# Performance work log

Hardware: AMD Instinct MI355X
Metric: run time of the kernel (lower is better)

Reference implementation:

```python
import jax, jax.numpy as jnp
import numpy as np

B, F, CTX, HID, L, NB = 16384, 64, 128, 512, 8, 2


def setup_inputs() -> dict:
    key = jax.random.key(0)
    ks = jax.random.split(key, 8)
    inputs = jax.random.normal(ks[0], (B, F), jnp.float32)
    context = jax.random.normal(ks[1], (B, CTX), jnp.float32)
    n_id = F // 2                      # identity features per coupling layer
    in_dim = n_id + CTX                # coupling net input = identity half + context
    out_dim = F                        # 2 * num_transform_features (shift | scale)
    s_in = 1.0 / np.sqrt(in_dim)
    s_h = 1.0 / np.sqrt(HID)
    W_in = jax.random.uniform(ks[2], (L, in_dim, HID), jnp.float32, -s_in, s_in)
    b_in = jax.random.uniform(ks[3], (L, HID), jnp.float32, -s_in, s_in)
    W_h = jax.random.uniform(ks[4], (L, NB, HID, HID), jnp.float32, -s_h, s_h)
    b_h = jax.random.uniform(ks[5], (L, NB, HID), jnp.float32, -s_h, s_h)
    # output layer init: normal(0, 0.01) weight, zero bias (as in torch source)
    W_out = 0.01 * jax.random.normal(ks[6], (L, HID, out_dim), jnp.float32)
    b_out = jnp.zeros((L, out_dim), jnp.float32)
    # fixed random permutations between coupling layers (nflows RandomPermutation buffers)
    rng = np.random.RandomState(42)
    perms = jnp.asarray(np.stack([rng.permutation(F) for _ in range(L - 1)]), jnp.int32)
    return dict(inputs=inputs, context=context, W_in=W_in, b_in=b_in,
                W_h=W_h, b_h=b_h, W_out=W_out, b_out=b_out, perms=perms)


def reference(inputs, context, W_in, b_in, W_h, b_h, W_out, b_out, perms):
    F_ = inputs.shape[-1]
    n_layers = W_in.shape[0]
    n_blocks = W_h.shape[1]
    nt = F_ // 2  # num transform features
    even_idx = jnp.arange(0, F_, 2)
    odd_idx = jnp.arange(1, F_, 2)
    x = jnp.clip(inputs, -1.0, 1.0)
    logdet = jnp.zeros(x.shape[0], x.dtype)
    for i in range(n_layers):
        # mask[::2]=1 for even layers -> mask>0 (even indices) are TRANSFORM features
        if i % 2 == 0:
            t_idx, id_idx = even_idx, odd_idx
        else:
            t_idx, id_idx = odd_idx, even_idx
        id_split = x[:, id_idx]   # [B, nt]
        tr_split = x[:, t_idx]    # [B, nt]
        h = jax.nn.relu(jnp.concatenate([id_split, context], -1) @ W_in[i] + b_in[i])
        for j in range(n_blocks):
            h = jax.nn.relu(h @ W_h[i, j] + b_h[i, j])
        p = h @ W_out[i] + b_out[i]            # [B, 2*nt]
        shift = p[:, :nt]
        scale = jax.nn.sigmoid(p[:, nt:] + 2.0) + 1e-3
        logdet = logdet + jnp.sum(jnp.log(scale), axis=-1)
        x = x.at[:, t_idx].set(tr_split * scale + shift).at[:, id_idx].set(id_split)
        if i < n_layers - 1:
            x = x[:, perms[i]]
    return jnp.clip(x, -1.0, 1.0), logdet
```

## Files before the change

### kernel.cpp

```cpp
#include <hip/hip_runtime.h>


typedef float v4f  __attribute__((ext_vector_type(4)));
typedef float v16f __attribute__((ext_vector_type(16)));
typedef int   v4i  __attribute__((ext_vector_type(4)));
typedef int   v8i  __attribute__((ext_vector_type(8)));
typedef unsigned char uchar;
typedef unsigned long long ull;

#define BATCH 16384
#define NF    64
#define NCTX  128
#define NL    8

#define RS     528
#define HHALF  256
#define AST    208
#define AHALF  96
#define PST    68

#define WSCALE     16.0f
#define WSCALE_INV 0.0625f

#define WIN_EPL   (192 * 512)
#define WH_EPB    (512 * 512)
#define WOUT_EPL  (512 * 64)
#define OFF_WIN   ((size_t)0)
#define OFF_WH    ((size_t)(8 * WIN_EPL))
#define OFF_WOUT  (OFF_WH + (size_t)(16 * WH_EPB))
#define TOT_PACK_ELEMS (OFF_WOUT + (size_t)(8 * WOUT_EPL))
#define NEED_WS   (TOT_PACK_ELEMS)

template<bool HI>
__device__ __forceinline__ unsigned int pk2(float a, float b, unsigned int old) {
    return __builtin_amdgcn_cvt_pk_fp8_f32(a, b, old, HI);
}
__device__ __forceinline__ uchar q8(float v) {
    return (uchar)(__builtin_amdgcn_cvt_pk_fp8_f32(v, v, 0u, false) & 0xffu);
}

__global__ void pack_weights_kernel(const float* __restrict__ W_in,
                                    const float* __restrict__ W_h,
                                    const float* __restrict__ W_out,
                                    unsigned char* __restrict__ ws) {
    const int TIN  = 8 * (WIN_EPL / 8);
    const int TH   = 16 * (WH_EPB / 8);
    const int TOUT = 8 * (WOUT_EPL / 8);
    int t = blockIdx.x * blockDim.x + threadIdx.x;
    if (t >= TIN + TH + TOUT) return;
    float v[8];
    if (t < TIN + TH) {
        const float* src; int r, rawK;
        if (t < TIN) {
            int i = t / (WIN_EPL / 8); r = t - i * (WIN_EPL / 8);
            src = W_in + (size_t)i * (160 * 512); rawK = 160;
        } else {
            int u = t - TIN; int ij = u >> 15; r = u & 32767;
            src = W_h + (size_t)ij * WH_EPB; rawK = 512;
        }
        int kb  = r >> 12, rem = r & 4095;
        int ls  = rem >> 2, g = rem & 3;
        int lane = ls & 63;
        int n = (ls >> 6) * 32 + (lane & 31);
        int pig = (g == 1) ? 2 : (g == 2) ? 1 : g;
        int k0 = kb * 64 + (lane >> 5) * 32 + pig * 8;
#pragma unroll
        for (int j = 0; j < 8; ++j) {
            int k = k0 + j;
            v[j] = (k < rawK) ? src[(size_t)k * 512 + n] * WSCALE : 0.f;
        }
    } else {
        int u = t - TIN - TH;
        int i = u >> 12, r = u & 4095;
        const float* src = W_out + (size_t)i * WOUT_EPL;
        int frag = r >> 6, lane = r & 63;
        int k0 = (frag >> 2) * 32 + (lane >> 4) * 8;
        int n  = (frag & 3) * 16 + (lane & 15);
#pragma unroll
        for (int j = 0; j < 8; ++j)
            v[j] = src[(size_t)(k0 + j) * 64 + n] * WSCALE;
    }
    uint2 o;
    o.x = pk2<false>(v[0], v[1], 0u);
    o.x = pk2<true >(v[2], v[3], o.x);
    o.y = pk2<false>(v[4], v[5], 0u);
    o.y = pk2<true >(v[6], v[7], o.y);
    *(uint2*)(ws + (size_t)t * 8) = o;
}

__device__ __forceinline__ v16f mfma32(ull a, ull b, v16f c) {
    return __builtin_amdgcn_mfma_f32_32x32x16_fp8_fp8((long)a, (long)b, c, 0, 0, 0);
}
__device__ __forceinline__ v4f mfma16(ull a, ull b, v4f c) {
    return __builtin_amdgcn_mfma_f32_16x16x32_fp8_fp8((long)a, (long)b, c, 0, 0, 0);
}
__device__ __forceinline__ v16f mfma64(v8i a, v8i b, v16f c) {
    return __builtin_amdgcn_mfma_scale_f32_32x32x64_f8f6f4(
        a, b, c, 0, 0, 0, 0x7f7f7f7f, 0, 0x7f7f7f7f);
}

template<int NKB>
__device__ __forceinline__ void gemm32mx(
    const uchar* __restrict__ wpk,
    const float* __restrict__ bias,
    const uchar* __restrict__ Abuf, int ast, int halfoff,
    uchar* __restrict__ Obuf,
    int pair, int lane)
{
    const int l31 = lane & 31, hl = lane >> 5;
    v16f a00, a01, a10, a11;
#pragma unroll
    for (int r = 0; r < 16; ++r) { a00[r] = 0.f; a01[r] = 0.f;
                                   a10[r] = 0.f; a11[r] = 0.f; }
    const uchar* aLo0 = Abuf + l31 * ast + hl * 16;
    const uchar* aHi0 = aLo0 + halfoff;
    const uchar* aLo1 = aLo0 + 32 * ast;
    const uchar* aHi1 = aHi0 + 32 * ast;
    const uchar* bp = wpk + (size_t)(pair * 128 + lane) * 32;

    auto loadB = [&](int s, int kb) -> v8i {
        if (kb >= NKB) kb = NKB - 1;
        const uchar* p = bp + s * 2048 + (size_t)kb * 32768;
        v4i lo = *(const v4i*)p;
        v4i hi = *(const v4i*)(p + 16);
        return __builtin_shufflevector(lo, hi, 0, 1, 2, 3, 4, 5, 6, 7);
    };
    auto loadA = [&](const uchar* lo_, const uchar* hi_, int kb) -> v8i {
        v4i lo = *(const v4i*)(lo_ + kb * 32);
        v4i hi = *(const v4i*)(hi_ + kb * 32);
        return __builtin_shufflevector(lo, hi, 0, 1, 2, 3, 4, 5, 6, 7);
    };

    v8i b00 = loadB(0, 0), b10 = loadB(1, 0);
    v8i b01 = loadB(0, 1), b11 = loadB(1, 1);
    int kb = 0;
#pragma unroll 1
    for (; kb + 1 < NKB; kb += 2) {
        v8i x0 = loadA(aLo0, aHi0, kb);
        v8i x1 = loadA(aLo1, aHi1, kb);
        a00 = mfma64(b00, x0, a00);
        a01 = mfma64(b00, x1, a01);
        a10 = mfma64(b10, x0, a10);
        a11 = mfma64(b10, x1, a11);
        b00 = loadB(0, kb + 2); b10 = loadB(1, kb + 2);
        x0 = loadA(aLo0, aHi0, kb + 1);
        x1 = loadA(aLo1, aHi1, kb + 1);
        a00 = mfma64(b01, x0, a00);
        a01 = mfma64(b01, x1, a01);
        a10 = mfma64(b11, x0, a10);
        a11 = mfma64(b11, x1, a11);
        b01 = loadB(0, kb + 3); b11 = loadB(1, kb + 3);
    }
    if constexpr (NKB & 1) {
        v8i x0 = loadA(aLo0, aHi0, NKB - 1);
        v8i x1 = loadA(aLo1, aHi1, NKB - 1);
        a00 = mfma64(b00, x0, a00);
        a01 = mfma64(b00, x1, a01);
        a10 = mfma64(b10, x0, a10);
        a11 = mfma64(b10, x1, a11);
    }

    const uchar* ob0 = Obuf + l31 * RS + 4 * hl;
    const uchar* ob1 = ob0 + 32 * RS;
    auto emit = [&](const v16f& am0, const v16f& am1, int strip) {
#pragma unroll
        for (int q = 0; q < 4; ++q) {
            const int n0 = strip * 32 + q * 8 + 4 * hl;
            float4 bv = *(const float4*)(bias + n0);
            unsigned int u0, u1;
            u0 = pk2<false>(fmaxf(fmaf(am0[4 * q + 0], WSCALE_INV, bv.x), 0.f),
                            fmaxf(fmaf(am0[4 * q + 1], WSCALE_INV, bv.y), 0.f), 0u);
            u0 = pk2<true >(fmaxf(fmaf(am0[4 * q + 2], WSCALE_INV, bv.z), 0.f),
                            fmaxf(fmaf(am0[4 * q + 3], WSCALE_INV, bv.w), 0.f), u0);
            u1 = pk2<false>(fmaxf(fmaf(am1[4 * q + 0], WSCALE_INV, bv.x), 0.f),
                            fmaxf(fmaf(am1[4 * q + 1], WSCALE_INV, bv.y), 0.f), 0u);
            u1 = pk2<true >(fmaxf(fmaf(am1[4 * q + 2], WSCALE_INV, bv.z), 0.f),
                            fmaxf(fmaf(am1[4 * q + 3], WSCALE_INV, bv.w), 0.f), u1);
            const int g = strip * 4 + q;
            const int off = (g & 1) * HHALF + ((g >> 1) << 3);
            *(unsigned int*)(ob0 + off) = u0;
            *(unsigned int*)(ob1 + off) = u1;
        }
    };
    emit(a00, a01, pair * 2 + 0);
    emit(a10, a11, pair * 2 + 1);
}

template<int KC>
__device__ __forceinline__ void gemm32_raw(
    const float* __restrict__ wraw,
    const float* __restrict__ bias,
    const uchar* __restrict__ Abuf, int ast, int ahalf,
    uchar* __restrict__ Obuf,
    int strip, int lane)
{
    constexpr int P = KC / 2;
    const int l31 = lane & 31, hl = lane >> 5;
    v16f acc0, acc1;
#pragma unroll
    for (int r = 0; r < 16; ++r) { acc0[r] = 0.f; acc1[r] = 0.f; }
    const uchar* a0p = Abuf + l31 * ast + hl * ahalf;
    const uchar* a1p = a0p + 32 * ast;

    auto loadB = [&](int kc) -> ull {
        if (kc >= KC) kc = KC - 1;
        int n  = strip * 32 + l31;
        int k0 = kc * 16 + hl * 8;
        unsigned int lo, hi;
        lo = pk2<false>(wraw[(size_t)(k0 + 0) * 512 + n] * WSCALE,
                        wraw[(size_t)(k0 + 1) * 512 + n] * WSCALE, 0u);
        lo = pk2<true >(wraw[(size_t)(k0 + 2) * 512 + n] * WSCALE,
                        wraw[(size_t)(k0 + 3) * 512 + n] * WSCALE, lo);
        hi = pk2<false>(wraw[(size_t)(k0 + 4) * 512 + n] * WSCALE,
                        wraw[(size_t)(k0 + 5) * 512 + n] * WSCALE, 0u);
        hi = pk2<true >(wraw[(size_t)(k0 + 6) * 512 + n] * WSCALE,
                        wraw[(size_t)(k0 + 7) * 512 + n] * WSCALE, hi);
        return ((ull)hi << 32) | (ull)lo;
    };

    ull b0 = loadB(0), b1 = loadB(1), b2 = loadB(2), b3 = loadB(3);
    int p2 = 0;
#pragma unroll 1
    for (; p2 + 1 < P; p2 += 2) {
        ulonglong2 Aa0 = *(const ulonglong2*)(a0p + p2 * 16);
        ulonglong2 Aa1 = *(const ulonglong2*)(a1p + p2 * 16);
        acc0 = mfma32(Aa0.x, b0, acc0);
        acc1 = mfma32(Aa1.x, b0, acc1);
        b0 = loadB(2 * p2 + 4);
        acc0 = mfma32(Aa0.y, b1, acc0);
        acc1 = mfma32(Aa1.y, b1, acc1);
        b1 = loadB(2 * p2 + 5);
        ulonglong2 Ab0 = *(const ulonglong2*)(a0p + p2 * 16 + 16);
        ulonglong2 Ab1 = *(const ulonglong2*)(a1p + p2 * 16 + 16);
        acc0 = mfma32(Ab0.x, b2, acc0);
        acc1 = mfma32(Ab1.x, b2, acc1);
        b2 = loadB(2 * p2 + 6);
        acc0 = mfma32(Ab0.y, b3, acc0);
        acc1 = mfma32(Ab1.y, b3, acc1);
        b3 = loadB(2 * p2 + 7);
    }
    if constexpr (P & 1) {
        ulonglong2 Aa0 = *(const ulonglong2*)(a0p + (P - 1) * 16);
        ulonglong2 Aa1 = *(const ulonglong2*)(a1p + (P - 1) * 16);
        acc0 = mfma32(Aa0.x, b0, acc0);
        acc1 = mfma32(Aa1.x, b0, acc1);
        acc0 = mfma32(Aa0.y, b1, acc0);
        acc1 = mfma32(Aa1.y, b1, acc1);
    }

    const int n = strip * 32 + l31;
    const int nb = ((n >> 3) & 1) * HHALF + ((n >> 4) << 3) + (n & 7);
    const float bv = bias[n];
#pragma unroll
    for (int reg = 0; reg < 16; ++reg) {
        int row = (reg & 3) + 8 * (reg >> 2) + 4 * hl;
        float v0 = fmaxf(fmaf(acc0[reg], WSCALE_INV, bv), 0.f);
        Obuf[row * RS + nb] = q8(v0);
        float v1 = fmaxf(fmaf(acc1[reg], WSCALE_INV, bv), 0.f);
        Obuf[(row + 32) * RS + nb] = q8(v1);
    }
}

template<bool PACKED>
__device__ __forceinline__ void gemm16_out(
    const uchar* __restrict__ wpk,
    const float* __restrict__ wraw,
    const float* __restrict__ bias,
    const uchar* __restrict__ Abuf,
    float* __restrict__ Pbuf,
    int w, int lane)
{
    const int quad = lane >> 4, l15 = lane & 15;
    const int ntb  = w & 3;
    const int mtb0 = w >> 2;
    const int row0 = mtb0 * 16 + l15;
    const int row1 = row0 + 32;
    v4f acc0, acc1;
    acc0[0] = acc0[1] = acc0[2] = acc0[3] = 0.f;
    acc1[0] = acc1[1] = acc1[2] = acc1[3] = 0.f;
    const uchar* ap0 = Abuf + row0 * RS + (quad & 1) * HHALF + ((quad >> 1) << 3);
    const uchar* ap1 = Abuf + row1 * RS + (quad & 1) * HHALF + ((quad >> 1) << 3);
    const uchar* bptr =
        PACKED ? wpk + (size_t)(ntb * 64 + lane) * 8 : (const uchar*)0;
    constexpr int KC = 16;

    auto loadB = [&](int kc) -> ull {
        if (kc >= KC) kc = KC - 1;
        if constexpr (PACKED) {
            return *(const ull*)(bptr + (size_t)kc * 2048);
        } else {
            int n  = ntb * 16 + l15;
            int k0 = kc * 32 + quad * 8;
            unsigned int lo, hi;
            lo = pk2<false>(wraw[(size_t)(k0 + 0) * 64 + n] * WSCALE,
                            wraw[(size_t)(k0 + 1) * 64 + n] * WSCALE, 0u);
            lo = pk2<true >(wraw[(size_t)(k0 + 2) * 64 + n] * WSCALE,
                            wraw[(size_t)(k0 + 3) * 64 + n] * WSCALE, lo);
            hi = pk2<false>(wraw[(size_t)(k0 + 4) * 64 + n] * WSCALE,
                            wraw[(size_t)(k0 + 5) * 64 + n] * WSCALE, 0u);
            hi = pk2<true >(wraw[(size_t)(k0 + 6) * 64 + n] * WSCALE,
                            wraw[(size_t)(k0 + 7) * 64 + n] * WSCALE, hi);
            return ((ull)hi << 32) | (ull)lo;
        }
    };
    auto step = [&](int kc, ull bb) {
        ull a0 = *(const ull*)(ap0 + kc * 16);
        acc0 = mfma16(bb, a0, acc0);
        ull a1 = *(const ull*)(ap1 + kc * 16);
        acc1 = mfma16(bb, a1, acc1);
    };

    ull b0 = loadB(0), b1 = loadB(1), b2 = loadB(2), b3 = loadB(3);
    int kc = 0;
#pragma unroll 1
    for (; kc + 3 < KC; kc += 4) {
        step(kc + 0, b0); b0 = loadB(kc + 4);
        step(kc + 1, b1); b1 = loadB(kc + 5);
        step(kc + 2, b2); b2 = loadB(kc + 6);
        step(kc + 3, b3); b3 = loadB(kc + 7);
    }

    float4 bv = *(const float4*)(bias + ntb * 16 + quad * 4);
    float4 o0, o1;
    o0.x = fmaf(acc0[0], WSCALE_INV, bv.x);
    o0.y = fmaf(acc0[1], WSCALE_INV, bv.y);
    o0.z = fmaf(acc0[2], WSCALE_INV, bv.z);
    o0.w = fmaf(acc0[3], WSCALE_INV, bv.w);
    *(float4*)(Pbuf + row0 * PST + ntb * 16 + quad * 4) = o0;
    o1.x = fmaf(acc1[0], WSCALE_INV, bv.x);
    o1.y = fmaf(acc1[1], WSCALE_INV, bv.y);
    o1.z = fmaf(acc1[2], WSCALE_INV, bv.z);
    o1.w = fmaf(acc1[3], WSCALE_INV, bv.w);
    *(float4*)(Pbuf + row1 * PST + ntb * 16 + quad * 4) = o1;
}

template<bool PACKED>
__global__ __launch_bounds__(512, 2) void flow_kernel(
    const float* __restrict__ inputs,
    const float* __restrict__ ctx,
    const float* __restrict__ W_in,  const float* __restrict__ b_in,
    const float* __restrict__ W_h,   const float* __restrict__ b_h,
    const float* __restrict__ W_out, const float* __restrict__ b_out,
    const int*   __restrict__ perms,
    const uchar* __restrict__ wpk,
    float* __restrict__ out)
{
    __shared__ __align__(16) uchar hbuf0[64 * RS];
    __shared__ __align__(16) uchar hbuf1[64 * RS];
    __shared__ __align__(16) uchar abuf[64 * AST];
    __shared__ __align__(16) float xbuf[64 * NF];
    __shared__ int permsh[NF];

    float* pbuf    = (float*)hbuf1;
    float* scratch = (float*)hbuf0;

    const int tid  = threadIdx.x;
    const int wave = tid >> 6;
    const int lane = tid & 63;
    const int trow = tid >> 3;
    const int t8   = tid & 7;
    const int row0 = blockIdx.x * 64;

    {
#pragma unroll
        for (int j = 0; j < 2; ++j) {
            float4 v = ((const float4*)(inputs + (size_t)row0 * NF))[tid + j * 512];
            v.x = fminf(fmaxf(v.x, -1.f), 1.f);
            v.y = fminf(fmaxf(v.y, -1.f), 1.f);
            v.z = fminf(fmaxf(v.z, -1.f), 1.f);
            v.w = fminf(fmaxf(v.w, -1.f), 1.f);
            ((float4*)xbuf)[tid + j * 512] = v;
        }
    }
    {
        const float* crow = ctx + (size_t)(row0 + trow) * NCTX + t8 * 16;
        float4 f0 = ((const float4*)crow)[0];
        float4 f1 = ((const float4*)crow)[1];
        float4 f2 = ((const float4*)crow)[2];
        float4 f3 = ((const float4*)crow)[3];
        uint2 ck0, ck1;
        ck0.x = pk2<false>(f0.x, f0.y, 0u);
        ck0.x = pk2<true >(f0.z, f0.w, ck0.x);
        ck0.y = pk2<false>(f1.x, f1.y, 0u);
        ck0.y = pk2<true >(f1.z, f1.w, ck0.y);
        ck1.x = pk2<false>(f2.x, f2.y, 0u);
        ck1.x = pk2<true >(f2.z, f2.w, ck1.x);
        ck1.y = pk2<false>(f3.x, f3.y, 0u);
        ck1.y = pk2<true >(f3.z, f3.w, ck1.y);
        *(uint2*)(abuf + trow * AST + (2 + t8) * 8) = ck0;
        *(uint2*)(abuf + trow * AST + AHALF + (2 + t8) * 8) = ck1;
    }
    if (tid < 256) {
        int r = tid >> 2, q = tid & 3;
        *(ull*)(abuf + r * AST + (q & 1) * AHALF + 80 + ((q >> 1) << 3)) = 0ULL;
    }
    float ld_acc = 0.f;
    __syncthreads();

#pragma unroll 1
    for (int i = 0; i < NL; ++i) {
        const int par = i & 1;
        const int idp = par ^ 1;

        if (t8 < 4) {
            const float* xr = xbuf + trow * NF + idp;
            uint2 idv;
            idv.x = pk2<false>(xr[2 * (t8 * 8 + 0)], xr[2 * (t8 * 8 + 1)], 0u);
            idv.x = pk2<true >(xr[2 * (t8 * 8 + 2)], xr[2 * (t8 * 8 + 3)], idv.x);
            idv.y = pk2<false>(xr[2 * (t8 * 8 + 4)], xr[2 * (t8 * 8 + 5)], 0u);
            idv.y = pk2<true >(xr[2 * (t8 * 8 + 6)], xr[2 * (t8 * 8 + 7)], idv.y);
            *(uint2*)(abuf + trow * AST + (t8 & 1) * AHALF + ((t8 >> 1) << 3)) = idv;
        }
        __syncthreads();

        if constexpr (PACKED) {
            gemm32mx<3>(wpk + OFF_WIN + (size_t)i * WIN_EPL, b_in + i * 512,
                        abuf, AST, AHALF, hbuf0, wave, lane);
            __syncthreads();
            gemm32mx<8>(wpk + OFF_WH + (size_t)(i * 2 + 0) * WH_EPB,
                        b_h + (i * 2 + 0) * 512,
                        hbuf0, RS, HHALF, hbuf1, wave, lane);
            __syncthreads();
            gemm32mx<8>(wpk + OFF_WH + (size_t)(i * 2 + 1) * WH_EPB,
                        b_h + (i * 2 + 1) * 512,
                        hbuf1, RS, HHALF, hbuf0, wave, lane);
            __syncthreads();
        } else {
            gemm32_raw<10>(W_in + (size_t)i * (160 * 512), b_in + i * 512,
                           abuf, AST, AHALF, hbuf0, wave * 2 + 0, lane);
            gemm32_raw<10>(W_in + (size_t)i * (160 * 512), b_in + i * 512,
                           abuf, AST, AHALF, hbuf0, wave * 2 + 1, lane);
            __syncthreads();
            gemm32_raw<32>(W_h + (size_t)(i * 2 + 0) * WH_EPB,
                           b_h + (i * 2 + 0) * 512,
                           hbuf0, RS, HHALF, hbuf1, wave * 2 + 0, lane);
            gemm32_raw<32>(W_h + (size_t)(i * 2 + 0) * WH_EPB,
                           b_h + (i * 2 + 0) * 512,
                           hbuf0, RS, HHALF, hbuf1, wave * 2 + 1, lane);
            __syncthreads();
            gemm32_raw<32>(W_h + (size_t)(i * 2 + 1) * WH_EPB,
                           b_h + (i * 2 + 1) * 512,
                           hbuf1, RS, HHALF, hbuf0, wave * 2 + 0, lane);
            gemm32_raw<32>(W_h + (size_t)(i * 2 + 1) * WH_EPB,
                           b_h + (i * 2 + 1) * 512,
                           hbuf1, RS, HHALF, hbuf0, wave * 2 + 1, lane);
            __syncthreads();
        }
        gemm16_out<PACKED>(
            PACKED ? wpk + OFF_WOUT + (size_t)i * WOUT_EPL : (const uchar*)0,
            W_out + (size_t)i * WOUT_EPL, b_out + i * 64,
            hbuf0, pbuf, wave, lane);
        __syncthreads();

        {
#pragma unroll
            for (int j = 0; j < 4; ++j) {
                int sc = t8 * 4 + j;
                float shiftv = pbuf[trow * PST + sc];
                float z = pbuf[trow * PST + 32 + sc] + 2.0f;
                float s = 1.0f / (1.0f + __expf(-z)) + 0.001f;
                int tc = 2 * sc + par;
                xbuf[trow * NF + tc] = xbuf[trow * NF + tc] * s + shiftv;
                ld_acc += __logf(s);
            }
        }
        __syncthreads();

        if (i < NL - 1) {
            ((float4*)scratch)[tid]       = ((float4*)xbuf)[tid];
            ((float4*)scratch)[tid + 512] = ((float4*)xbuf)[tid + 512];
            if (tid < NF) permsh[tid] = perms[i * NF + tid];
            __syncthreads();
#pragma unroll
            for (int j = 0; j < 8; ++j) {
                int c = t8 * 8 + j;
                xbuf[trow * NF + c] = scratch[trow * NF + permsh[c]];
            }
            __syncthreads();
        }
    }

    {
#pragma unroll
        for (int j = 0; j < 2; ++j) {
            float4 v = ((float4*)xbuf)[tid + j * 512];
            v.x = fminf(fmaxf(v.x, -1.f), 1.f);
            v.y = fminf(fmaxf(v.y, -1.f), 1.f);
            v.z = fminf(fmaxf(v.z, -1.f), 1.f);
            v.w = fminf(fmaxf(v.w, -1.f), 1.f);
            ((float4*)(out + (size_t)row0 * NF))[tid + j * 512] = v;
        }
    }
    ld_acc += __shfl_down(ld_acc, 1);
    ld_acc += __shfl_down(ld_acc, 2);
    ld_acc += __shfl_down(ld_acc, 4);
    if (t8 == 0) out[(size_t)BATCH * NF + row0 + trow] = ld_acc;
}

extern "C" void kernel_launch(void* const* d_in, const int* in_sizes, int n_in,
                              void* d_out, int out_size, void* d_ws, size_t ws_size,
                              hipStream_t stream) {
    const float* inputs  = (const float*)d_in[0];
    const float* context = (const float*)d_in[1];
    const float* W_in    = (const float*)d_in[2];
    const float* b_in    = (const float*)d_in[3];
    const float* W_h     = (const float*)d_in[4];
    const float* b_h     = (const float*)d_in[5];
    const float* W_out   = (const float*)d_in[6];
    const float* b_out   = (const float*)d_in[7];
    const int*   perms   = (const int*)d_in[8];
    float* out = (float*)d_out;

    if (ws_size >= (size_t)NEED_WS) {
        uchar* ws = (uchar*)d_ws;
        const int total_threads = (int)(TOT_PACK_ELEMS / 8);
        pack_weights_kernel<<<(total_threads + 255) / 256, 256, 0, stream>>>(
            W_in, W_h, W_out, ws);
        flow_kernel<true><<<256, 512, 0, stream>>>(
            inputs, context, W_in, b_in, W_h, b_h, W_out, b_out, perms, ws, out);
    } else {
        flow_kernel<false><<<256, 512, 0, stream>>>(
            inputs, context, W_in, b_in, W_h, b_h, W_out, b_out, perms,
            (const uchar*)0, out);
    }
}
```

Measured before the change: 200.3 us.

## Fuse affine coupling epilogue into output GEMM and replace permutations with composed index table

The output GEMM is restructured so each wave computes both the shift and scale tiles for the same rows, which lets it apply the sigmoid, the affine update and the log-determinant directly in registers instead of staging them through a shared buffer. The per-layer physical permutation of xbuf (copy to scratch, gather back, two barriers) is removed. In its place a table of composed permutation indices, built once per block, is used for indirect reads and writes into xbuf. This removes several barriers and shared-memory passes per layer, at the cost of irregular gathers into xbuf and a table-building loop of up to seven chained global reads at startup.

```diff
diff --git a/kernel.cpp b/kernel.cpp
--- a/kernel.cpp
+++ b/kernel.cpp
@@ -17,7 +17,6 @@
 #define HHALF  256
 #define AST    208
 #define AHALF  96
-#define PST    68
 
 #define WSCALE     16.0f
 #define WSCALE_INV 0.0625f
@@ -262,32 +261,34 @@
 }
 
 template<bool PACKED>
-__device__ __forceinline__ void gemm16_out(
+__device__ __forceinline__ float gemm16_fused(
     const uchar* __restrict__ wpk,
     const float* __restrict__ wraw,
     const float* __restrict__ bias,
     const uchar* __restrict__ Abuf,
-    float* __restrict__ Pbuf,
-    int w, int lane)
+    float* __restrict__ xbuf,
+    const int* __restrict__ ct,
+    int par, int w, int lane)
 {
     const int quad = lane >> 4, l15 = lane & 15;
-    const int ntb  = w & 3;
-    const int mtb0 = w >> 2;
-    const int row0 = mtb0 * 16 + l15;
-    const int row1 = row0 + 32;
+    const int mtb  = w >> 1;
+    const int npair = w & 1;
+    const int ntb0 = npair, ntb1 = npair + 2;
+    const int row  = mtb * 16 + l15;
     v4f acc0, acc1;
     acc0[0] = acc0[1] = acc0[2] = acc0[3] = 0.f;
     acc1[0] = acc1[1] = acc1[2] = acc1[3] = 0.f;
-    const uchar* ap0 = Abuf + row0 * RS + (quad & 1) * HHALF + ((quad >> 1) << 3);
-    const uchar* ap1 = Abuf + row1 * RS + (quad & 1) * HHALF + ((quad >> 1) << 3);
-    const uchar* bptr =
-        PACKED ? wpk + (size_t)(ntb * 64 + lane) * 8 : (const uchar*)0;
+    const uchar* ap = Abuf + row * RS + (quad & 1) * HHALF + ((quad >> 1) << 3);
+    const uchar* bp0 =
+        PACKED ? wpk + (size_t)(ntb0 * 64 + lane) * 8 : (const uchar*)0;
+    const uchar* bp1 =
+        PACKED ? wpk + (size_t)(ntb1 * 64 + lane) * 8 : (const uchar*)0;
     constexpr int KC = 16;
 
-    auto loadB = [&](int kc) -> ull {
+    auto loadB = [&](const uchar* bp, int ntb, int kc) -> ull {
         if (kc >= KC) kc = KC - 1;
         if constexpr (PACKED) {
-            return *(const ull*)(bptr + (size_t)kc * 2048);
+            return *(const ull*)(bp + (size_t)kc * 2048);
         } else {
             int n  = ntb * 16 + l15;
             int k0 = kc * 32 + quad * 8;
@@ -303,35 +304,43 @@
             return ((ull)hi << 32) | (ull)lo;
         }
     };
-    auto step = [&](int kc, ull bb) {
-        ull a0 = *(const ull*)(ap0 + kc * 16);
-        acc0 = mfma16(bb, a0, acc0);
-        ull a1 = *(const ull*)(ap1 + kc * 16);
-        acc1 = mfma16(bb, a1, acc1);
+    auto step = [&](int kc, ull bu, ull bv_) {
+        ull a = *(const ull*)(ap + kc * 16);
+        acc0 = mfma16(bu, a, acc0);
+        acc1 = mfma16(bv_, a, acc1);
     };
 
-    ull b0 = loadB(0), b1 = loadB(1), b2 = loadB(2), b3 = loadB(3);
+    ull u0 = loadB(bp0, ntb0, 0), u1 = loadB(bp0, ntb0, 1);
+    ull u2 = loadB(bp0, ntb0, 2), u3 = loadB(bp0, ntb0, 3);
+    ull v0 = loadB(bp1, ntb1, 0), v1 = loadB(bp1, ntb1, 1);
+    ull v2 = loadB(bp1, ntb1, 2), v3 = loadB(bp1, ntb1, 3);
     int kc = 0;
 #pragma unroll 1
     for (; kc + 3 < KC; kc += 4) {
-        step(kc + 0, b0); b0 = loadB(kc + 4);
-        step(kc + 1, b1); b1 = loadB(kc + 5);
-        step(kc + 2, b2); b2 = loadB(kc + 6);
-        step(kc + 3, b3); b3 = loadB(kc + 7);
-    }
-
-    float4 bv = *(const float4*)(bias + ntb * 16 + quad * 4);
-    float4 o0, o1;
-    o0.x = fmaf(acc0[0], WSCALE_INV, bv.x);
-    o0.y = fmaf(acc0[1], WSCALE_INV, bv.y);
-    o0.z = fmaf(acc0[2], WSCALE_INV, bv.z);
-    o0.w = fmaf(acc0[3], WSCALE_INV, bv.w);
-    *(float4*)(Pbuf + row0 * PST + ntb * 16 + quad * 4) = o0;
-    o1.x = fmaf(acc1[0], WSCALE_INV, bv.x);
-    o1.y = fmaf(acc1[1], WSCALE_INV, bv.y);
-    o1.z = fmaf(acc1[2], WSCALE_INV, bv.z);
-    o1.w = fmaf(acc1[3], WSCALE_INV, bv.w);
-    *(float4*)(Pbuf + row1 * PST + ntb * 16 + quad * 4) = o1;
+        step(kc + 0, u0, v0);
+        u0 = loadB(bp0, ntb0, kc + 4); v0 = loadB(bp1, ntb1, kc + 4);
+        step(kc + 1, u1, v1);
+        u1 = loadB(bp0, ntb0, kc + 5); v1 = loadB(bp1, ntb1, kc + 5);
+        step(kc + 2, u2, v2);
+        u2 = loadB(bp0, ntb0, kc + 6); v2 = loadB(bp1, ntb1, kc + 6);
+        step(kc + 3, u3, v3);
+        u3 = loadB(bp0, ntb0, kc + 7); v3 = loadB(bp1, ntb1, kc + 7);
+    }
+
+    const int n0 = ntb0 * 16 + quad * 4;
+    float ld = 0.f;
+#pragma unroll
+    for (int r = 0; r < 4; ++r) {
+        float shiftv = fmaf(acc0[r], WSCALE_INV, bias[n0 + r]);
+        float z      = fmaf(acc1[r], WSCALE_INV, bias[32 + n0 + r]) + 2.0f;
+        float s      = 1.0f / (1.0f + __expf(-z)) + 0.001f;
+        int sc = n0 + r;
+        int tc = ct[2 * sc + par];
+        float xo = xbuf[row * NF + tc];
+        xbuf[row * NF + tc] = xo * s + shiftv;
+        ld += __logf(s);
+    }
+    return ld;
 }
 
 template<bool PACKED>
@@ -349,10 +358,7 @@
     __shared__ __align__(16) uchar hbuf1[64 * RS];
     __shared__ __align__(16) uchar abuf[64 * AST];
     __shared__ __align__(16) float xbuf[64 * NF];
-    __shared__ int permsh[NF];
-
-    float* pbuf    = (float*)hbuf1;
-    float* scratch = (float*)hbuf0;
+    __shared__ int Ctab[NL * NF];
 
     const int tid  = threadIdx.x;
     const int wave = tid >> 6;
@@ -361,6 +367,12 @@
     const int t8   = tid & 7;
     const int row0 = blockIdx.x * 64;
 
+    {
+        int i = tid >> 6, c = tid & 63;
+        int idx = c;
+        for (int k = i - 1; k >= 0; --k) idx = perms[k * NF + idx];
+        Ctab[tid] = idx;
+    }
     {
 #pragma unroll
         for (int j = 0; j < 2; ++j) {
@@ -401,14 +413,19 @@
     for (int i = 0; i < NL; ++i) {
         const int par = i & 1;
         const int idp = par ^ 1;
+        const int* ct = Ctab + i * NF;
 
         if (t8 < 4) {
-            const float* xr = xbuf + trow * NF + idp;
+            const float* xr = xbuf + trow * NF;
             uint2 idv;
-            idv.x = pk2<false>(xr[2 * (t8 * 8 + 0)], xr[2 * (t8 * 8 + 1)], 0u);
-            idv.x = pk2<true >(xr[2 * (t8 * 8 + 2)], xr[2 * (t8 * 8 + 3)], idv.x);
-            idv.y = pk2<false>(xr[2 * (t8 * 8 + 4)], xr[2 * (t8 * 8 + 5)], 0u);
-            idv.y = pk2<true >(xr[2 * (t8 * 8 + 6)], xr[2 * (t8 * 8 + 7)], idv.y);
+            idv.x = pk2<false>(xr[ct[2 * (t8 * 8 + 0) + idp]],
+                               xr[ct[2 * (t8 * 8 + 1) + idp]], 0u);
+            idv.x = pk2<true >(xr[ct[2 * (t8 * 8 + 2) + idp]],
+                               xr[ct[2 * (t8 * 8 + 3) + idp]], idv.x);
+            idv.y = pk2<false>(xr[ct[2 * (t8 * 8 + 4) + idp]],
+                               xr[ct[2 * (t8 * 8 + 5) + idp]], 0u);
+            idv.y = pk2<true >(xr[ct[2 * (t8 * 8 + 6) + idp]],
+                               xr[ct[2 * (t8 * 8 + 7) + idp]], idv.y);
             *(uint2*)(abuf + trow * AST + (t8 & 1) * AHALF + ((t8 >> 1) << 3)) = idv;
         }
         __syncthreads();
@@ -446,55 +463,41 @@
                            hbuf1, RS, HHALF, hbuf0, wave * 2 + 1, lane);
             __syncthreads();
         }
-        gemm16_out<PACKED>(
+        ld_acc += gemm16_fused<PACKED>(
             PACKED ? wpk + OFF_WOUT + (size_t)i * WOUT_EPL : (const uchar*)0,
             W_out + (size_t)i * WOUT_EPL, b_out + i * 64,
-            hbuf0, pbuf, wave, lane);
+            hbuf0, xbuf, ct, par, wave, lane);
         __syncthreads();
-
-        {
-#pragma unroll
-            for (int j = 0; j < 4; ++j) {
-                int sc = t8 * 4 + j;
-                float shiftv = pbuf[trow * PST + sc];
-                float z = pbuf[trow * PST + 32 + sc] + 2.0f;
-                float s = 1.0f / (1.0f + __expf(-z)) + 0.001f;
-                int tc = 2 * sc + par;
-                xbuf[trow * NF + tc] = xbuf[trow * NF + tc] * s + shiftv;
-                ld_acc += __logf(s);
-            }
-        }
+    }
+
+    {
+        const int* c7 = Ctab + 7 * NF;
+#pragma unroll
+        for (int j = 0; j < 2; ++j) {
+            int p = tid + j * 512;
+            int r = p >> 4, c0 = (p & 15) * 4;
+            const float* xr = xbuf + r * NF;
+            float4 v;
+            v.x = fminf(fmaxf(xr[c7[c0 + 0]], -1.f), 1.f);
+            v.y = fminf(fmaxf(xr[c7[c0 + 1]], -1.f), 1.f);
+            v.z = fminf(fmaxf(xr[c7[c0 + 2]], -1.f), 1.f);
+            v.w = fminf(fmaxf(xr[c7[c0 + 3]], -1.f), 1.f);
+            ((float4*)(out + (size_t)row0 * NF))[p] = v;
+        }
+    }
+    {
+        float* lbuf = (float*)abuf;
+        const int rrow = (wave >> 1) * 16 + (lane & 15);
+        const int slot = (wave & 1) * 4 + (lane >> 4);
+        lbuf[rrow * 8 + slot] = ld_acc;
         __syncthreads();
-
-        if (i < NL - 1) {
-            ((float4*)scratch)[tid]       = ((float4*)xbuf)[tid];
-            ((float4*)scratch)[tid + 512] = ((float4*)xbuf)[tid + 512];
-            if (tid < NF) permsh[tid] = perms[i * NF + tid];
-            __syncthreads();
-#pragma unroll
-            for (int j = 0; j < 8; ++j) {
-                int c = t8 * 8 + j;
-                xbuf[trow * NF + c] = scratch[trow * NF + permsh[c]];
-            }
-            __syncthreads();
-        }
-    }
-
-    {
-#pragma unroll
-        for (int j = 0; j < 2; ++j) {
-            float4 v = ((float4*)xbuf)[tid + j * 512];
-            v.x = fminf(fmaxf(v.x, -1.f), 1.f);
-            v.y = fminf(fmaxf(v.y, -1.f), 1.f);
-            v.z = fminf(fmaxf(v.z, -1.f), 1.f);
-            v.w = fminf(fmaxf(v.w, -1.f), 1.f);
-            ((float4*)(out + (size_t)row0 * NF))[tid + j * 512] = v;
-        }
-    }
-    ld_acc += __shfl_down(ld_acc, 1);
-    ld_acc += __shfl_down(ld_acc, 2);
-    ld_acc += __shfl_down(ld_acc, 4);
-    if (t8 == 0) out[(size_t)BATCH * NF + row0 + trow] = ld_acc;
+        if (tid < 64) {
+            float s = 0.f;
+#pragma unroll
+            for (int k = 0; k < 8; ++k) s += lbuf[tid * 8 + k];
+            out[(size_t)BATCH * NF + row0 + tid] = s;
+        }
+    }
 }
 
 extern "C" void kernel_launch(void* const* d_in, const int* in_sizes, int n_in,
```

Result: no change. 198.9 us (-0.7%).
